# Performance work log

Hardware: AMD Instinct MI355X
Metric: run time of the kernel (lower is better)

## Reference

```python
import jax, jax.numpy as jnp
import numpy as np

N, K, D = 200000, 16, 64


def setup_inputs() -> dict:
    key = jax.random.key(0)
    k1, k2, k3, k4 = jax.random.split(key, 4)
    X = jax.random.normal(k1, (N, D), dtype=jnp.float32)
    pi = jax.nn.softmax(jax.random.normal(k2, (K,), dtype=jnp.float32))
    mus = jax.random.normal(k3, (K, D), dtype=jnp.float32)
    # build SPD covariance matrices: A A^T + 0.5 I
    A = 0.1 * jax.random.normal(k4, (K, D, D), dtype=jnp.float32)
    covs = jnp.einsum('kij,klj->kil', A, A) + 0.5 * jnp.eye(D, dtype=jnp.float32)[None]
    return {"X": X, "pi": pi, "mus": mus, "covs": covs}


def reference(X, pi, mus, covs):
    # GaussianMixtureModel.estimate_log_prob: per-component MVN log_prob + logsumexp
    # fused into one batched Cholesky/Mahalanobis computation.
    d = X.shape[1]
    L = jnp.linalg.cholesky(covs)                      # [K, D, D]
    diff = X[None, :, :] - mus[:, None, :]             # [K, N, D]
    # solve L z = diff^T per component -> whitened residuals
    solve = jax.vmap(lambda Lk, dk: jax.scipy.linalg.solve_triangular(Lk, dk.T, lower=True))
    z = solve(L, diff)                                 # [K, D, N]
    maha = jnp.sum(z * z, axis=1)                      # [K, N]
    half_logdet = jnp.sum(jnp.log(jnp.diagonal(L, axis1=1, axis2=2)), axis=1)  # [K]
    log2pi = jnp.asarray(np.log(2.0 * np.pi), dtype=X.dtype)
    log_prob = -0.5 * (d * log2pi + maha) - half_logdet[:, None]   # [K, N]
    weighted = jnp.log(pi)[:, None] + log_prob          # [K, N]
    # stable softmax over components == exp(weighted - logsumexp)
    r_E = jax.nn.softmax(weighted, axis=0).T            # [N, K]
    return r_E
```

## Files before the change

### kernel.cpp

```cpp
#include <hip/hip_runtime.h>
#include <cstddef>
#include <cstdint>


#define GMM_D 64
#define GMM_K 16

typedef _Float16 half8 __attribute__((ext_vector_type(8)));
typedef float f32x4 __attribute__((ext_vector_type(4)));

#define WA_BYTES (GMM_K * 16 * 64 * 8 * 2)

__device__ __forceinline__ float fast_rsqrt(float x) {
#if __has_builtin(__builtin_amdgcn_rsqf)
    const float r = __builtin_amdgcn_rsqf(x);
    return r * (1.5f - 0.5f * x * r * r);
#else
    return 1.0f / sqrtf(x);
#endif
}

__device__ __forceinline__ float lane_bcast(float v, int l) {
    return __int_as_float(__builtin_amdgcn_readlane(__float_as_int(v), l));
}

__global__ __launch_bounds__(64) void gmm_precompute_kernel(
    const float* __restrict__ pi, const float* __restrict__ mus,
    const float* __restrict__ covs, _Float16* __restrict__ WA,
    float* __restrict__ tv, float* __restrict__ cc)
{
    const int k = blockIdx.x;
    const int r = threadIdx.x;

    __shared__ alignas(16) float Ls[GMM_D][68];
    __shared__ float Wv[GMM_D][GMM_D + 1];

    float A_r[GMM_D];
    {
        const float4* src = reinterpret_cast<const float4*>(
            covs + (size_t)k * GMM_D * GMM_D + (size_t)r * GMM_D);
        #pragma unroll
        for (int u = 0; u < GMM_D / 4; ++u) {
            const float4 v = src[u];
            A_r[4 * u + 0] = v.x; A_r[4 * u + 1] = v.y;
            A_r[4 * u + 2] = v.z; A_r[4 * u + 3] = v.w;
        }
    }

    float mydiag = 1.0f, myrs = 1.0f;
    #pragma unroll
    for (int j = 0; j < GMM_D; ++j) {
        const float pivot = lane_bcast(A_r[j], j);
        const float rs = fast_rsqrt(pivot);
        const float valj = A_r[j] * rs;
        if (r == j) { mydiag = valj; myrs = rs; }
        A_r[j] = valj;
        #pragma unroll
        for (int p = j + 1; p < GMM_D; ++p)
            A_r[p] -= valj * lane_bcast(valj, p);
    }

    #pragma unroll
    for (int p = 0; p < GMM_D; ++p)
        Ls[r][p] = (p <= r) ? A_r[p] : 0.0f;
    __syncthreads();

    float w[GMM_D];
    #pragma unroll
    for (int i = 0; i < GMM_D; ++i) w[i] = 0.0f;

    #pragma unroll
    for (int i = 0; i < GMM_D; ++i) {
        const f32x4* Lrow = reinterpret_cast<const f32x4*>(&Ls[i][0]);
        float a0 = 0.0f, a1 = 0.0f, a2 = 0.0f, a3 = 0.0f;
        #pragma unroll
        for (int u = 0; u <= (i >> 2); ++u) {
            const f32x4 lv = Lrow[u];
            a0 -= lv[0] * w[4 * u + 0];
            a1 -= lv[1] * w[4 * u + 1];
            a2 -= lv[2] * w[4 * u + 2];
            a3 -= lv[3] * w[4 * u + 3];
        }
        const float invd = lane_bcast(myrs, i);
        const float dlt = (r == i) ? 1.0f : 0.0f;
        w[i] = (dlt + (a0 + a1) + (a2 + a3)) * invd;
    }

    #pragma unroll
    for (int i = 0; i < GMM_D; ++i)
        Wv[i][r] = w[i];
    __syncthreads();

    {
        const float* mk = mus + k * GMM_D;
        float s0 = 0.f, s1 = 0.f, s2 = 0.f, s3 = 0.f;
        #pragma unroll
        for (int c = 0; c < GMM_D; c += 4) {
            s0 += Wv[r][c + 0] * mk[c + 0];
            s1 += Wv[r][c + 1] * mk[c + 1];
            s2 += Wv[r][c + 2] * mk[c + 2];
            s3 += Wv[r][c + 3] * mk[c + 3];
        }
        tv[k * GMM_D + r] = -((s0 + s1) + (s2 + s3));
    }

    {
        const int lr = r & 15, q = r >> 4;
        #pragma unroll
        for (int f = 0; f < 16; ++f) {
            const int mt = f >> 2, s = f & 3;
            const int row = mt * 16 + lr;
            const int db = (s & 1) * 32 + q * 8;
            half8 hv;
            #pragma unroll
            for (int u = 0; u < 8; ++u) {
                const float v = Wv[row][db + u];
                _Float16 h = (_Float16)v;
                if (s >= 2) h = (_Float16)(v - (float)h);
                hv[u] = h;
            }
            *(half8*)(WA + ((size_t)((k * 16 + f) * 64) + r) * 8) = hv;
        }
    }

    {
        float ll = logf(mydiag);
        #pragma unroll
        for (int off = 32; off > 0; off >>= 1) ll += __shfl_down(ll, off);
        if (r == 0)
            cc[k] = logf(pi[k]) - ll - 0.5f * 64.0f * 1.8378770664093453f;
    }
}

__global__ __launch_bounds__(256) void gmm_estep_kernel(
    const float* __restrict__ X, const _Float16* __restrict__ WA,
    const float* __restrict__ tv, const float* __restrict__ cc,
    float* __restrict__ out, int N)
{
    __shared__ _Float16 xs[64 * 136];
    __shared__ float lg[64 * 17];

    const int tid = threadIdx.x;

    {
        const int p = tid >> 2, qq = tid & 3;
        const int np = blockIdx.x * 64 + p;
        if (np < N) {
            const float4* src = reinterpret_cast<const float4*>(X + (size_t)np * GMM_D) + qq * 4;
            float vv[16];
            #pragma unroll
            for (int u = 0; u < 4; ++u) {
                const float4 v = src[u];
                vv[4 * u + 0] = v.x; vv[4 * u + 1] = v.y;
                vv[4 * u + 2] = v.z; vv[4 * u + 3] = v.w;
            }
            half8 h0, h1, l0, l1;
            #pragma unroll
            for (int u = 0; u < 8; ++u) {
                const _Float16 a = (_Float16)vv[u];
                const _Float16 b = (_Float16)vv[u + 8];
                h0[u] = a; l0[u] = (_Float16)(vv[u] - (float)a);
                h1[u] = b; l1[u] = (_Float16)(vv[u + 8] - (float)b);
            }
            _Float16* row = xs + p * 136;
            *(half8*)(row + qq * 16)          = h0;
            *(half8*)(row + qq * 16 + 8)      = h1;
            *(half8*)(row + 64 + qq * 16)     = l0;
            *(half8*)(row + 64 + qq * 16 + 8) = l1;
        }
    }
    __syncthreads();

    const int lane = tid & 63;
    const int wave = __builtin_amdgcn_readfirstlane(tid >> 6);
    const int pt = lane & 15;
    const int q  = lane >> 4;

    #pragma unroll 1
    for (int kk = 0; kk < 4; ++kk) {
        const int k = wave * 4 + kk;

        half8 af[4][4];
        const _Float16* wab = WA + (size_t)k * 8192 + lane * 8;
        #pragma unroll
        for (int mt = 0; mt < 4; ++mt)
            #pragma unroll
            for (int s = 0; s < 4; ++s)
                af[mt][s] = *(const half8*)(wab + (mt * 4 + s) * 512);

        f32x4 tk4[4];
        #pragma unroll
        for (int mt = 0; mt < 4; ++mt)
            tk4[mt] = *(const f32x4*)(tv + k * 64 + mt * 16 + q * 4);

        #pragma unroll 1
        for (int nt = 0; nt < 4; ++nt) {
            const _Float16* xrow = xs + (nt * 16 + pt) * 136 + q * 8;
            const half8 bh0 = *(const half8*)(xrow);
            const half8 bh1 = *(const half8*)(xrow + 32);
            const half8 bl0 = *(const half8*)(xrow + 64);
            const half8 bl1 = *(const half8*)(xrow + 96);

            float mahaP = 0.0f;
            #pragma unroll
            for (int mt = 0; mt < 4; ++mt) {
                f32x4 c = tk4[mt];
                c = __builtin_amdgcn_mfma_f32_16x16x32_f16(af[mt][0], bh0, c, 0, 0, 0);
                c = __builtin_amdgcn_mfma_f32_16x16x32_f16(af[mt][1], bh1, c, 0, 0, 0);
                c = __builtin_amdgcn_mfma_f32_16x16x32_f16(af[mt][0], bl0, c, 0, 0, 0);
                c = __builtin_amdgcn_mfma_f32_16x16x32_f16(af[mt][1], bl1, c, 0, 0, 0);
                c = __builtin_amdgcn_mfma_f32_16x16x32_f16(af[mt][2], bh0, c, 0, 0, 0);
                c = __builtin_amdgcn_mfma_f32_16x16x32_f16(af[mt][3], bh1, c, 0, 0, 0);
                mahaP += c[0] * c[0] + c[1] * c[1] + c[2] * c[2] + c[3] * c[3];
            }
            mahaP += __shfl_xor(mahaP, 16);
            mahaP += __shfl_xor(mahaP, 32);
            if (q == 0 && (blockIdx.x * 64 + nt * 16 + pt) < N)
                lg[(nt * 16 + pt) * 17 + k] = cc[k] - 0.5f * mahaP;
        }
    }
    __syncthreads();

    {
        const int p = tid >> 2, qq = tid & 3;
        const int np = blockIdx.x * 64 + p;
        if (np < N) {
            const float* row = &lg[p * 17];
            float m = row[0];
            #pragma unroll
            for (int j = 1; j < GMM_K; ++j) m = fmaxf(m, row[j]);
            float e[GMM_K];
            float s = 0.0f;
            #pragma unroll
            for (int j = 0; j < GMM_K; ++j) { e[j] = __expf(row[j] - m); s += e[j]; }
            const float inv = 1.0f / s;
            float4 v;
            v.x = e[qq * 4 + 0] * inv;
            v.y = e[qq * 4 + 1] * inv;
            v.z = e[qq * 4 + 2] * inv;
            v.w = e[qq * 4 + 3] * inv;
            reinterpret_cast<float4*>(out + (size_t)np * GMM_K)[qq] = v;
        }
    }
}

extern "C" void kernel_launch(void* const* d_in, const int* in_sizes, int n_in,
                              void* d_out, int out_size, void* d_ws, size_t ws_size,
                              hipStream_t stream)
{
    const float* X    = (const float*)d_in[0];
    const float* pi   = (const float*)d_in[1];
    const float* mus  = (const float*)d_in[2];
    const float* covs = (const float*)d_in[3];
    float* out = (float*)d_out;

    const int N = in_sizes[0] / GMM_D;

    _Float16* WA = (_Float16*)d_ws;
    float* tv = (float*)((char*)d_ws + WA_BYTES);
    float* cc = tv + GMM_K * GMM_D;

    gmm_precompute_kernel<<<dim3(GMM_K), dim3(64), 0, stream>>>(pi, mus, covs, WA, tv, cc);

    const int blocks = (N + 63) / 64;
    gmm_estep_kernel<<<dim3(blocks), dim3(256), 0, stream>>>(X, WA, tv, cc, out, N);
}
```

Measured before the change: 176.0 us.

## Switch Mahalanobis MFMA from 16x16x32 to 32x32x16 tiles with matching layouts

Reworks the whitening GEMM to use 32x32x16 f16 MFMA instructions instead of 16x16x32. The precomputed whitening-matrix fragments and bias vector are re-laid out to match the new accumulator layout. The per-point reduction now needs only one cross-lane shuffle instead of two, and s_setprio is raised around the MFMA chain. The larger tiles are meant to cut instruction count and operand reloads per FLOP, at the cost of more accumulator registers per wave.

```diff
diff --git a/kernel.cpp b/kernel.cpp
--- a/kernel.cpp
+++ b/kernel.cpp
@@ -8,6 +8,7 @@
 
 typedef _Float16 half8 __attribute__((ext_vector_type(8)));
 typedef float f32x4 __attribute__((ext_vector_type(4)));
+typedef float f32x16 __attribute__((ext_vector_type(16)));
 
 #define WA_BYTES (GMM_K * 16 * 64 * 8 * 2)
 
@@ -101,23 +102,25 @@
             s2 += Wv[r][c + 2] * mk[c + 2];
             s3 += Wv[r][c + 3] * mk[c + 3];
         }
-        tv[k * GMM_D + r] = -((s0 + s1) + (s2 + s3));
-    }
-
-    {
-        const int lr = r & 15, q = r >> 4;
+        const int idx = (r >> 5) * 32 + ((r >> 2) & 1) * 16
+                      + (r & 3) + 4 * ((r >> 3) & 3);
+        tv[k * GMM_D + idx] = -((s0 + s1) + (s2 + s3));
+    }
+
+    {
+        const int lr = r & 31, g = r >> 5;
         #pragma unroll
         for (int f = 0; f < 16; ++f) {
-            const int mt = f >> 2, s = f & 3;
-            const int row = mt * 16 + lr;
-            const int db = (s & 1) * 32 + q * 8;
+            const int mt = f >> 3, ks = (f >> 1) & 3, h = f & 1;
+            const int row = mt * 32 + lr;
+            const int db = ks * 16 + g * 8;
             half8 hv;
             #pragma unroll
             for (int u = 0; u < 8; ++u) {
                 const float v = Wv[row][db + u];
-                _Float16 h = (_Float16)v;
-                if (s >= 2) h = (_Float16)(v - (float)h);
-                hv[u] = h;
+                _Float16 hh = (_Float16)v;
+                if (h) hh = (_Float16)(v - (float)hh);
+                hv[u] = hh;
             }
             *(half8*)(WA + ((size_t)((k * 16 + f) * 64) + r) * 8) = hv;
         }
@@ -173,50 +176,72 @@
 
     const int lane = tid & 63;
     const int wave = __builtin_amdgcn_readfirstlane(tid >> 6);
-    const int pt = lane & 15;
-    const int q  = lane >> 4;
+    const int pt32 = lane & 31;
+    const int g    = lane >> 5;
 
     #pragma unroll 1
     for (int kk = 0; kk < 4; ++kk) {
         const int k = wave * 4 + kk;
 
-        half8 af[4][4];
+        half8 af[2][4][2];
         const _Float16* wab = WA + (size_t)k * 8192 + lane * 8;
         #pragma unroll
-        for (int mt = 0; mt < 4; ++mt)
-            #pragma unroll
-            for (int s = 0; s < 4; ++s)
-                af[mt][s] = *(const half8*)(wab + (mt * 4 + s) * 512);
-
-        f32x4 tk4[4];
-        #pragma unroll
-        for (int mt = 0; mt < 4; ++mt)
-            tk4[mt] = *(const f32x4*)(tv + k * 64 + mt * 16 + q * 4);
+        for (int mt = 0; mt < 2; ++mt)
+            #pragma unroll
+            for (int ks = 0; ks < 4; ++ks)
+                #pragma unroll
+                for (int h = 0; h < 2; ++h)
+                    af[mt][ks][h] = *(const half8*)(wab + (mt * 8 + ks * 2 + h) * 512);
+
+        f32x16 t16[2];
+        #pragma unroll
+        for (int mt = 0; mt < 2; ++mt)
+            t16[mt] = *(const f32x16*)(tv + k * 64 + mt * 32 + g * 16);
 
         #pragma unroll 1
-        for (int nt = 0; nt < 4; ++nt) {
-            const _Float16* xrow = xs + (nt * 16 + pt) * 136 + q * 8;
-            const half8 bh0 = *(const half8*)(xrow);
-            const half8 bh1 = *(const half8*)(xrow + 32);
-            const half8 bl0 = *(const half8*)(xrow + 64);
-            const half8 bl1 = *(const half8*)(xrow + 96);
-
-            float mahaP = 0.0f;
-            #pragma unroll
-            for (int mt = 0; mt < 4; ++mt) {
-                f32x4 c = tk4[mt];
-                c = __builtin_amdgcn_mfma_f32_16x16x32_f16(af[mt][0], bh0, c, 0, 0, 0);
-                c = __builtin_amdgcn_mfma_f32_16x16x32_f16(af[mt][1], bh1, c, 0, 0, 0);
-                c = __builtin_amdgcn_mfma_f32_16x16x32_f16(af[mt][0], bl0, c, 0, 0, 0);
-                c = __builtin_amdgcn_mfma_f32_16x16x32_f16(af[mt][1], bl1, c, 0, 0, 0);
-                c = __builtin_amdgcn_mfma_f32_16x16x32_f16(af[mt][2], bh0, c, 0, 0, 0);
-                c = __builtin_amdgcn_mfma_f32_16x16x32_f16(af[mt][3], bh1, c, 0, 0, 0);
-                mahaP += c[0] * c[0] + c[1] * c[1] + c[2] * c[2] + c[3] * c[3];
-            }
-            mahaP += __shfl_xor(mahaP, 16);
+        for (int nt = 0; nt < 2; ++nt) {
+            const _Float16* xrow = xs + (nt * 32 + pt32) * 136 + g * 8;
+            half8 bh[4];
+            #pragma unroll
+            for (int ks = 0; ks < 4; ++ks)
+                bh[ks] = *(const half8*)(xrow + ks * 16);
+
+            __builtin_amdgcn_s_setprio(1);
+            f32x16 c0 = __builtin_amdgcn_mfma_f32_32x32x16_f16(af[0][0][0], bh[0], t16[0], 0, 0, 0);
+            f32x16 c1 = __builtin_amdgcn_mfma_f32_32x32x16_f16(af[1][0][0], bh[0], t16[1], 0, 0, 0);
+            #pragma unroll
+            for (int ks = 1; ks < 4; ++ks) {
+                c0 = __builtin_amdgcn_mfma_f32_32x32x16_f16(af[0][ks][0], bh[ks], c0, 0, 0, 0);
+                c1 = __builtin_amdgcn_mfma_f32_32x32x16_f16(af[1][ks][0], bh[ks], c1, 0, 0, 0);
+            }
+            #pragma unroll
+            for (int ks = 0; ks < 4; ++ks) {
+                c0 = __builtin_amdgcn_mfma_f32_32x32x16_f16(af[0][ks][1], bh[ks], c0, 0, 0, 0);
+                c1 = __builtin_amdgcn_mfma_f32_32x32x16_f16(af[1][ks][1], bh[ks], c1, 0, 0, 0);
+            }
+            half8 bl[4];
+            #pragma unroll
+            for (int ks = 0; ks < 4; ++ks)
+                bl[ks] = *(const half8*)(xrow + 64 + ks * 16);
+            #pragma unroll
+            for (int ks = 0; ks < 4; ++ks) {
+                c0 = __builtin_amdgcn_mfma_f32_32x32x16_f16(af[0][ks][0], bl[ks], c0, 0, 0, 0);
+                c1 = __builtin_amdgcn_mfma_f32_32x32x16_f16(af[1][ks][0], bl[ks], c1, 0, 0, 0);
+            }
+            __builtin_amdgcn_s_setprio(0);
+
+            float s0 = 0.f, s1 = 0.f, s2 = 0.f, s3 = 0.f;
+            #pragma unroll
+            for (int u = 0; u < 16; u += 4) {
+                s0 += c0[u + 0] * c0[u + 0] + c1[u + 0] * c1[u + 0];
+                s1 += c0[u + 1] * c0[u + 1] + c1[u + 1] * c1[u + 1];
+                s2 += c0[u + 2] * c0[u + 2] + c1[u + 2] * c1[u + 2];
+                s3 += c0[u + 3] * c0[u + 3] + c1[u + 3] * c1[u + 3];
+            }
+            float mahaP = (s0 + s1) + (s2 + s3);
             mahaP += __shfl_xor(mahaP, 32);
-            if (q == 0 && (blockIdx.x * 64 + nt * 16 + pt) < N)
-                lg[(nt * 16 + pt) * 17 + k] = cc[k] - 0.5f * mahaP;
+            if (g == 0 && (blockIdx.x * 64 + nt * 32 + pt32) < N)
+                lg[(nt * 32 + pt32) * 17 + k] = cc[k] - 0.5f * mahaP;
         }
     }
     __syncthreads();
```

Result: slower. 193.1 us (+9.7%).

## Split waves by point tile instead of component, streaming weights per component

Applied to the files above, without the earlier changes.

Each wave now owns a 16-point tile and loops over all 16 components, instead of owning 4 components and looping over 4 point tiles. The point fragments (hi/lo fp16 splits) are loaded from shared memory once per wave, and the whitening-matrix fragments are fetched per component rather than held as a 16-register set reused across point tiles. This cuts register pressure and LDS reads of X, at the cost of each wave reading all components' weights from global memory/cache, which is 4x more weight traffic per block.

```diff
diff --git a/kernel.cpp b/kernel.cpp
--- a/kernel.cpp
+++ b/kernel.cpp
@@ -175,49 +175,40 @@
     const int wave = __builtin_amdgcn_readfirstlane(tid >> 6);
     const int pt = lane & 15;
     const int q  = lane >> 4;
+    const int prow = wave * 16 + pt;
+    const int np_l = blockIdx.x * 64 + prow;
+
+    const _Float16* xrow = xs + prow * 136 + q * 8;
+    const half8 bh0 = *(const half8*)(xrow);
+    const half8 bh1 = *(const half8*)(xrow + 32);
+    const half8 bl0 = *(const half8*)(xrow + 64);
+    const half8 bl1 = *(const half8*)(xrow + 96);
 
     #pragma unroll 1
-    for (int kk = 0; kk < 4; ++kk) {
-        const int k = wave * 4 + kk;
-
-        half8 af[4][4];
+    for (int k = 0; k < GMM_K; ++k) {
         const _Float16* wab = WA + (size_t)k * 8192 + lane * 8;
-        #pragma unroll
-        for (int mt = 0; mt < 4; ++mt)
-            #pragma unroll
-            for (int s = 0; s < 4; ++s)
-                af[mt][s] = *(const half8*)(wab + (mt * 4 + s) * 512);
-
-        f32x4 tk4[4];
-        #pragma unroll
-        for (int mt = 0; mt < 4; ++mt)
-            tk4[mt] = *(const f32x4*)(tv + k * 64 + mt * 16 + q * 4);
-
-        #pragma unroll 1
-        for (int nt = 0; nt < 4; ++nt) {
-            const _Float16* xrow = xs + (nt * 16 + pt) * 136 + q * 8;
-            const half8 bh0 = *(const half8*)(xrow);
-            const half8 bh1 = *(const half8*)(xrow + 32);
-            const half8 bl0 = *(const half8*)(xrow + 64);
-            const half8 bl1 = *(const half8*)(xrow + 96);
-
-            float mahaP = 0.0f;
-            #pragma unroll
-            for (int mt = 0; mt < 4; ++mt) {
-                f32x4 c = tk4[mt];
-                c = __builtin_amdgcn_mfma_f32_16x16x32_f16(af[mt][0], bh0, c, 0, 0, 0);
-                c = __builtin_amdgcn_mfma_f32_16x16x32_f16(af[mt][1], bh1, c, 0, 0, 0);
-                c = __builtin_amdgcn_mfma_f32_16x16x32_f16(af[mt][0], bl0, c, 0, 0, 0);
-                c = __builtin_amdgcn_mfma_f32_16x16x32_f16(af[mt][1], bl1, c, 0, 0, 0);
-                c = __builtin_amdgcn_mfma_f32_16x16x32_f16(af[mt][2], bh0, c, 0, 0, 0);
-                c = __builtin_amdgcn_mfma_f32_16x16x32_f16(af[mt][3], bh1, c, 0, 0, 0);
-                mahaP += c[0] * c[0] + c[1] * c[1] + c[2] * c[2] + c[3] * c[3];
-            }
-            mahaP += __shfl_xor(mahaP, 16);
-            mahaP += __shfl_xor(mahaP, 32);
-            if (q == 0 && (blockIdx.x * 64 + nt * 16 + pt) < N)
-                lg[(nt * 16 + pt) * 17 + k] = cc[k] - 0.5f * mahaP;
-        }
+        const float* tvk = tv + k * GMM_D;
+
+        float mahaP = 0.0f;
+        #pragma unroll
+        for (int mt = 0; mt < 4; ++mt) {
+            const half8 a0 = *(const half8*)(wab + (mt * 4 + 0) * 512);
+            const half8 a1 = *(const half8*)(wab + (mt * 4 + 1) * 512);
+            const half8 a2 = *(const half8*)(wab + (mt * 4 + 2) * 512);
+            const half8 a3 = *(const half8*)(wab + (mt * 4 + 3) * 512);
+            f32x4 c = *(const f32x4*)(tvk + mt * 16 + q * 4);
+            c = __builtin_amdgcn_mfma_f32_16x16x32_f16(a0, bh0, c, 0, 0, 0);
+            c = __builtin_amdgcn_mfma_f32_16x16x32_f16(a1, bh1, c, 0, 0, 0);
+            c = __builtin_amdgcn_mfma_f32_16x16x32_f16(a0, bl0, c, 0, 0, 0);
+            c = __builtin_amdgcn_mfma_f32_16x16x32_f16(a1, bl1, c, 0, 0, 0);
+            c = __builtin_amdgcn_mfma_f32_16x16x32_f16(a2, bh0, c, 0, 0, 0);
+            c = __builtin_amdgcn_mfma_f32_16x16x32_f16(a3, bh1, c, 0, 0, 0);
+            mahaP += c[0] * c[0] + c[1] * c[1] + c[2] * c[2] + c[3] * c[3];
+        }
+        mahaP += __shfl_xor(mahaP, 16);
+        mahaP += __shfl_xor(mahaP, 32);
+        if (q == 0 && np_l < N)
+            lg[prow * 17 + k] = cc[k] - 0.5f * mahaP;
     }
     __syncthreads();
 
```

After: 238.5 us. +35.5%, slower.
